# Kernel optimization log

Measured on AMD Instinct MI355X. Metric: run time of the kernel, lower is better.

Reference implementation:

```python
import jax, jax.numpy as jnp
import numpy as np

EMB, CLS, M_MARGIN, B = 512, 20000, 4, 256
LAMB = 1500.0 / 1.1          # AngleLoss lambda at it=1: max(5, 1500/(1+0.1*1))
LMD_INTER = 0.01
PI = 3.14159265              # constant used in original sphereface code


def setup_inputs() -> dict:
    key = jax.random.key(0)
    k1, k2, k3 = jax.random.split(key, 3)
    emb = jax.random.normal(k1, (B, EMB), dtype=jnp.float32)
    y = jax.random.randint(k2, (B,), 0, CLS)
    # weight initialized uniform(-1,1) then column-renormalized inside forward
    W = jax.random.uniform(k3, (EMB, CLS), dtype=jnp.float32, minval=-1.0, maxval=1.0)
    return {"emb": emb, "y": y, "W": W}


def _forward(emb, W, y):
    b = emb.shape[0]
    # --- ASoftmax (sphereface AngleLinear, m=4, phiflag=True) ---
    nm_W = W / jnp.linalg.norm(W, axis=0, keepdims=True)            # unit columns [E,C]
    xlen = jnp.linalg.norm(emb, axis=1, keepdims=True)              # [B,1]
    cos = jnp.clip((emb @ nm_W) / xlen, -1.0, 1.0)                  # [B,C]
    cos_m = 8.0 * cos**4 - 8.0 * cos**2 + 1.0                        # cos(4*theta)
    theta = jnp.arccos(jax.lax.stop_gradient(cos))                   # torch: acos on .data
    k = jnp.floor(M_MARGIN * theta / PI)
    sign = 1.0 - 2.0 * jnp.mod(k, 2.0)                               # (-1)^k
    phi = sign * cos_m - 2.0 * k
    cos_s = cos * xlen                                               # logits[0]
    phi_s = phi * xlen
    # --- AngleLoss (gamma=0) ---
    f = 1.0 / (1.0 + LAMB)
    onehot = jax.nn.one_hot(y, CLS, dtype=cos_s.dtype)               # [B,C]
    output = cos_s + onehot * f * (phi_s - cos_s)
    logpt = jax.nn.log_softmax(output, axis=1)
    logpt_t = jnp.take_along_axis(logpt, y[:, None], axis=1)[:, 0]
    ce = -jnp.mean(logpt_t)
    # --- MHE inter-class loss: sum_{i, j != y_i} 1/||w_{y_i} - w_j||^2 ---
    # unit columns => ||w_a - w_b||^2 = 2 - 2 <w_a, w_b>; avoids the
    # [E, B*C] scatter/repeat intermediate of the original.
    ws = nm_W[:, y]                                                  # [E,B]
    cosWW = ws.T @ nm_W                                              # [B,C]
    dist2 = jnp.maximum(2.0 - 2.0 * cosWW, 0.0)
    mask = onehot > 0.5                                              # j == y_i (z_n == 0)
    inv = jnp.where(mask, 0.0, 1.0 / jnp.where(mask, 1.0, dist2))
    inter = jnp.sum(inv) / (b * (CLS - 1))
    loss = ce + LMD_INTER * inter
    return loss, cos_s, inter


def reference(emb, y, W):
    loss, logits0, inter = _forward(emb, W, y)
    pred = jnp.argmax(logits0, axis=1)
    acc = jnp.mean((pred == y).astype(jnp.float32))
    return loss, logits0, acc, inter
```

## Files before the change

### kernel.cpp

```cpp
#include <hip/hip_runtime.h>
#include <hip/hip_bf16.h>
#include <math.h>

#define B_N   256
#define EMB_N 512
#define CLS_N 20000
#define CLS_PAD 20096
#define NMB   157
#define PI_F  3.14159265f
#define F_CONST ((float)(1.1 / 1501.1))

typedef __bf16 bf16x8 __attribute__((ext_vector_type(8)));
typedef float  f32x4  __attribute__((ext_vector_type(4)));

__device__ __forceinline__ unsigned short f2bf(float f) {
    unsigned u = __float_as_uint(f);
    unsigned r = (u + 0x7FFFu + ((u >> 16) & 1u)) >> 16;
    return (unsigned short)r;
}

__device__ __forceinline__ void merge4(float& M, float& S, float& VM, int& VI,
                                       float m2, float s2, float vm2, int vi2) {
    float mn = fmaxf(M, m2);
    if (mn == -INFINITY) { S = 0.f; }
    else S = S * __expf(M - mn) + s2 * __expf(m2 - mn);
    M = mn;
    if (vm2 > VM || (vm2 == VM && vi2 < VI)) { VM = vm2; VI = vi2; }
}

__device__ __forceinline__ int m204_wgid(int orig) {
    int xcd = orig & 7;
    return (xcd < 4 ? xcd * 79 : 316 + (xcd - 4) * 78) + (orig >> 3);
}

__global__ __launch_bounds__(256) void prep_convert_kernel(
    const float* __restrict__ emb, const int* __restrict__ y,
    const float* __restrict__ W,
    unsigned short* __restrict__ Abf, unsigned short* __restrict__ Wt,
    float* __restrict__ colsumsq4,
    float* __restrict__ xlen_a, float* __restrict__ inv_xlen_a,
    float* __restrict__ inv_wny_a, float* __restrict__ mod_val_a,
    float* __restrict__ accums)
{
    __shared__ alignas(16) unsigned short T[128][136];
    __shared__ float sSq[8][128];
    const int t = threadIdx.x;

    if (blockIdx.x < 628) {
        const int wgid = m204_wgid(blockIdx.x);
        const int c0 = (wgid >> 2) * 128;
        const int k0 = (wgid & 3) * 128;
        const int cl = (t & 31) * 4;
        const int kr = t >> 5;
        const int xp = (t & 7) << 3;
        float ssq[4] = {0.f, 0.f, 0.f, 0.f};

        #pragma unroll 4
        for (int it = 0; it < 16; ++it) {
            int k = k0 + it * 8 + kr;
            int c = c0 + cl;
            float4 v;
            if (c + 3 < CLS_N) {
                v = *reinterpret_cast<const float4*>(&W[(size_t)k * CLS_N + c]);
            } else {
                v.x = (c + 0 < CLS_N) ? W[(size_t)k * CLS_N + c + 0] : 0.f;
                v.y = (c + 1 < CLS_N) ? W[(size_t)k * CLS_N + c + 1] : 0.f;
                v.z = (c + 2 < CLS_N) ? W[(size_t)k * CLS_N + c + 2] : 0.f;
                v.w = (c + 3 < CLS_N) ? W[(size_t)k * CLS_N + c + 3] : 0.f;
            }
            float vv[4] = {v.x, v.y, v.z, v.w};
            int ki = ((it * 8) ^ xp) + kr;
            #pragma unroll
            for (int j = 0; j < 4; ++j) {
                ssq[j] += vv[j] * vv[j];
                T[cl + j][ki] = f2bf(vv[j]);
            }
        }
        #pragma unroll
        for (int j = 0; j < 4; ++j) sSq[kr][cl + j] = 0.f;
        __syncthreads();
        #pragma unroll
        for (int j = 0; j < 4; ++j) atomicAdd(&sSq[kr][cl + j], ssq[j]);
        __syncthreads();
        if (t < 128) {
            float s = 0.f;
            #pragma unroll
            for (int g = 0; g < 8; ++g) s += sSq[g][t];
            colsumsq4[(size_t)(wgid & 3) * CLS_PAD + c0 + t] = s;
        }
        for (int p = 0; p < 8; ++p) {
            int c  = p * 16 + (t >> 4);
            int xr = ((c >> 2) & 7) << 3;
            uint4 d = *reinterpret_cast<const uint4*>(&T[c][((t & 15) * 8) ^ xr]);
            *reinterpret_cast<uint4*>(&Wt[(size_t)(c0 + c) * EMB_N + k0 + (t & 15) * 8]) = d;
        }
    } else {
        float* r0 = (float*)T;
        float* r1 = r0 + 256;
        float* r2 = r0 + 512;
        const int b = blockIdx.x - 628;
        if (b == 0 && t < 4) accums[t] = 0.f;
        const int yb = y[b];
        const float* erow = emb + (size_t)b * EMB_N;
        float se = 0.f, sw = 0.f, dt = 0.f;
        for (int e = t; e < EMB_N; e += 256) {
            float ev = erow[e];
            float wv = W[(size_t)e * CLS_N + yb];
            Abf[(size_t)b * EMB_N + e]         = f2bf(ev);
            Abf[(size_t)(B_N + b) * EMB_N + e] = f2bf(wv);
            se += ev * ev; sw += wv * wv; dt += ev * wv;
        }
        r0[t] = se; r1[t] = sw; r2[t] = dt;
        __syncthreads();
        for (int s = 128; s > 0; s >>= 1) {
            if (t < s) { r0[t] += r0[t + s]; r1[t] += r1[t + s]; r2[t] += r2[t + s]; }
            __syncthreads();
        }
        if (t == 0) {
            float xlen = sqrtf(r0[0]);
            float wn   = sqrtf(r1[0]);
            float inv_x = 1.f / xlen;
            float inv_w = 1.f / wn;
            float cos_t = r2[0] * inv_w * inv_x;
            cos_t = fminf(1.f, fmaxf(-1.f, cos_t));
            float c2 = cos_t * cos_t;
            float cos_m = 8.f * c2 * c2 - 8.f * c2 + 1.f;
            float theta = acosf(cos_t);
            float k = floorf(4.f * theta / PI_F);
            float sgn = 1.f - 2.f * fmodf(k, 2.f);
            float phi = sgn * cos_m - 2.f * k;
            float cos_s = cos_t * xlen;
            float phi_s = phi * xlen;
            xlen_a[b] = xlen;
            inv_xlen_a[b] = inv_x;
            inv_wny_a[b] = inv_w;
            mod_val_a[b] = cos_s + F_CONST * (phi_s - cos_s);
        }
    }
}

__global__ __launch_bounds__(256, 3) void mfma_gemm_kernel(
    const unsigned short* __restrict__ Wt, const unsigned short* __restrict__ Abf,
    const float* __restrict__ colsumsq4, const int* __restrict__ y,
    const float* __restrict__ xlen_a, const float* __restrict__ inv_xlen_a,
    const float* __restrict__ inv_wny_a,
    float* __restrict__ logits, float4* __restrict__ partials,
    float* __restrict__ inter_sum)
{
    __shared__ alignas(16) char smem[49152];
    float*  sIwc  = (float*)smem;
    float4* sPart = (float4*)(smem + 512);
    float*  red   = (float*)(smem + 4608);

    const int wgid = m204_wgid(blockIdx.x);
    const int tile  = wgid >> 2;
    const int slice = wgid & 3;
    const int m0    = tile * 128;
    const int gn0   = slice * 128;

    const int t    = threadIdx.x;
    const int lane = t & 63;
    const int wid  = t >> 6;
    const int wr   = wid >> 1;
    const int wc   = wid & 1;
    const int r16  = lane & 15;
    const int kh   = lane >> 4;

    const char* Ab = (const char*)Wt;
    const char* Bb = (const char*)Abf;

    f32x4 acc[4][4] = {};

    const int srow = lane >> 2;
    const int srcq = (lane & 3) ^ ((lane >> 2) & 3);

    #define ISSUE_STEP(kt, slab)                                                  \
        { _Pragma("unroll")                                                       \
          for (int i = 0; i < 2; ++i) {                                           \
              int slot = wid * 2 + i;                                             \
              int row  = slot * 16 + srow;                                        \
              __builtin_amdgcn_global_load_lds(                                   \
                  (const __attribute__((address_space(1))) unsigned int*)         \
                      (Ab + (size_t)(m0 + row) * 1024                             \
                          + (size_t)(kt) * 2 + srcq * 16),                        \
                  (__attribute__((address_space(3))) unsigned int*)               \
                      (smem + (slab) * 8192 + slot * 1024),                       \
                  16, 0, 0);                                                      \
              __builtin_amdgcn_global_load_lds(                                   \
                  (const __attribute__((address_space(1))) unsigned int*)         \
                      (Bb + (size_t)(gn0 + row) * 1024                            \
                          + (size_t)(kt) * 2 + srcq * 16),                        \
                  (__attribute__((address_space(3))) unsigned int*)               \
                      (smem + 24576 + (slab) * 8192 + slot * 1024),               \
                  16, 0, 0);                                                      \
          } }

    #define COMPUTE(slab)                                                         \
        { bf16x8 af[4], bfr[4];                                                   \
          _Pragma("unroll")                                                       \
          for (int mi = 0; mi < 4; ++mi) {                                        \
              int row = wr * 64 + mi * 16 + r16;                                  \
              af[mi] = *reinterpret_cast<const bf16x8*>(                          \
                  smem + (slab) * 8192 + row * 64 + ((kh ^ (row & 3)) << 4));     \
          }                                                                       \
          _Pragma("unroll")                                                       \
          for (int ni = 0; ni < 4; ++ni) {                                        \
              int rowb = wc * 64 + ni * 16 + r16;                                 \
              bfr[ni] = *reinterpret_cast<const bf16x8*>(                         \
                  smem + 24576 + (slab) * 8192 + rowb * 64                        \
                  + ((kh ^ (rowb & 3)) << 4));                                    \
          }                                                                       \
          __builtin_amdgcn_s_setprio(1);                                          \
          _Pragma("unroll")                                                       \
          for (int mi = 0; mi < 4; ++mi)                                          \
              _Pragma("unroll")                                                   \
              for (int ni = 0; ni < 4; ++ni)                                      \
                  acc[mi][ni] = __builtin_amdgcn_mfma_f32_16x16x32_bf16(          \
                      af[mi], bfr[ni], acc[mi][ni], 0, 0, 0);                     \
          __builtin_amdgcn_s_setprio(0); }

    #define FENCE() __builtin_amdgcn_sched_barrier(0);

    ISSUE_STEP(0, 0)

    #pragma unroll
    for (int tt = 0; tt < 16; ++tt) {
        if (tt < 15) {
            ISSUE_STEP((tt + 1) * 32, (tt + 1) % 3)
            FENCE()
            asm volatile("s_waitcnt vmcnt(4)" ::: "memory");
        } else {
            FENCE()
            asm volatile("s_waitcnt vmcnt(0)" ::: "memory");
        }
        FENCE()
        asm volatile("s_barrier" ::: "memory");
        FENCE()
        COMPUTE(tt % 3)
        FENCE()
    }
    #undef ISSUE_STEP
    #undef COMPUTE
    #undef FENCE

    __syncthreads();

    if (t < 128) {
        int c = m0 + t;
        float s = colsumsq4[c] + colsumsq4[CLS_PAD + c]
                + colsumsq4[2 * CLS_PAD + c] + colsumsq4[3 * CLS_PAD + c];
        sIwc[t] = rsqrtf(s);
    }
    __syncthreads();

    float iwc[4][4];
    #pragma unroll
    for (int mi = 0; mi < 4; ++mi)
        #pragma unroll
        for (int r = 0; r < 4; ++r)
            iwc[mi][r] = sIwc[wr * 64 + mi * 16 + kh * 4 + r];

    if (slice < 2) {
        #pragma unroll
        for (int ni = 0; ni < 4; ++ni) {
            int bl = wc * 64 + ni * 16 + r16;
            int b  = gn0 + bl;
            float xl  = xlen_a[b];
            float ixl = inv_xlen_a[b];
            float M = -INFINITY, S = 0.f, VM = -INFINITY; int VI = 0x7fffffff;
            #pragma unroll
            for (int mi = 0; mi < 4; ++mi) {
                int cb = m0 + wr * 64 + mi * 16 + kh * 4;
                if (cb < CLS_N) {
                    f32x4 vout;
                    #pragma unroll
                    for (int r = 0; r < 4; ++r) {
                        float cosv = acc[mi][ni][r] * iwc[mi][r] * ixl;
                        cosv = fminf(1.f, fmaxf(-1.f, cosv));
                        float v = cosv * xl;
                        vout[r] = v;
                        if (v > M) { S = S * __expf(M - v) + 1.f; M = v; }
                        else       { S += __expf(v - M); }
                        if (v > VM) { VM = v; VI = cb + r; }
                    }
                    *reinterpret_cast<f32x4*>(&logits[(size_t)b * CLS_N + cb]) = vout;
                }
            }
            #pragma unroll
            for (int d = 16; d < 64; d <<= 1) {
                float m2  = __shfl_xor(M, d);
                float s2  = __shfl_xor(S, d);
                float vm2 = __shfl_xor(VM, d);
                int   vi2 = __shfl_xor(VI, d);
                merge4(M, S, VM, VI, m2, s2, vm2, vi2);
            }
            if (kh == 0) sPart[bl * 2 + wr] = make_float4(M, S, VM, __int_as_float(VI));
        }
        __syncthreads();
        if (t < 128) {
            float4 p0 = sPart[t * 2 + 0], p1 = sPart[t * 2 + 1];
            float M = p0.x, S = p0.y, VM = p0.z; int VI = __float_as_int(p0.w);
            merge4(M, S, VM, VI, p1.x, p1.y, p1.z, __float_as_int(p1.w));
            partials[(size_t)(gn0 + t) * NMB + tile] =
                make_float4(M, S, VM, __int_as_float(VI));
        }
    } else {
        float part = 0.f;
        #pragma unroll
        for (int ni = 0; ni < 4; ++ni) {
            int b = (slice - 2) * 128 + wc * 64 + ni * 16 + r16;
            float iwy = inv_wny_a[b];
            int   yb  = y[b];
            #pragma unroll
            for (int mi = 0; mi < 4; ++mi) {
                int cb = m0 + wr * 64 + mi * 16 + kh * 4;
                #pragma unroll
                for (int r = 0; r < 4; ++r) {
                    int c = cb + r;
                    if (c < CLS_N && c != yb) {
                        float cww = acc[mi][ni][r] * iwc[mi][r] * iwy;
                        float d2 = fmaxf(2.f - 2.f * cww, 0.f);
                        part += 1.f / d2;
                    }
                }
            }
        }
        red[t] = part;
        __syncthreads();
        for (int s = 128; s > 0; s >>= 1) {
            if (t < s) red[t] += red[t + s];
            __syncthreads();
        }
        if (t == 0) atomicAdd(inter_sum, red[0]);
    }
}

__global__ __launch_bounds__(64) void reduce_kernel(
    const float4* __restrict__ partials, const float* __restrict__ logits,
    const int* __restrict__ y, const float* __restrict__ mod_val_a,
    float* __restrict__ accums, float* __restrict__ out)
{
    const int b = blockIdx.x;
    const int t = threadIdx.x;
    float M = -INFINITY, S = 0.f, VM = -INFINITY; int VI = 0x7fffffff;
    for (int i = t; i < NMB; i += 64) {
        float4 p = partials[(size_t)b * NMB + i];
        merge4(M, S, VM, VI, p.x, p.y, p.z, __float_as_int(p.w));
    }
    #pragma unroll
    for (int d = 1; d < 64; d <<= 1) {
        float m2  = __shfl_xor(M, d);
        float s2  = __shfl_xor(S, d);
        float vm2 = __shfl_xor(VM, d);
        int   vi2 = __shfl_xor(VI, d);
        merge4(M, S, VM, VI, m2, s2, vm2, vi2);
    }
    if (t == 0) {
        int   yb  = y[b];
        float vyb = logits[(size_t)b * CLS_N + yb];
        float mv  = mod_val_a[b];
        float m2 = fmaxf(M, mv);
        float s2 = S * __expf(M - m2) - __expf(vyb - m2) + __expf(mv - m2);
        float lse = m2 + logf(s2);
        atomicAdd(&accums[0], -(mv - lse));
        if (VI == yb) atomicAdd(&accums[1], 1.f);
        __threadfence();
        int old = atomicAdd((int*)&accums[3], 1);
        if (old == B_N - 1) {
            float ce    = atomicAdd(&accums[0], 0.f) / (float)B_N;
            float acc   = atomicAdd(&accums[1], 0.f) / (float)B_N;
            float inter = atomicAdd(&accums[2], 0.f) / (float)((double)B_N * (CLS_N - 1));
            out[0] = ce + 0.01f * inter;
            out[(size_t)1 + (size_t)B_N * CLS_N + 0] = acc;
            out[(size_t)1 + (size_t)B_N * CLS_N + 1] = inter;
        }
    }
}

extern "C" void kernel_launch(void* const* d_in, const int* in_sizes, int n_in,
                              void* d_out, int out_size, void* d_ws, size_t ws_size,
                              hipStream_t stream) {
    const float* emb = (const float*)d_in[0];
    const int*   y   = (const int*)d_in[1];
    const float* W   = (const float*)d_in[2];
    float* out = (float*)d_out;
    float* logits = out + 1;

    const size_t ABF_OFF  = 0;
    const size_t WT_OFF   = 524288;
    const size_t CS_OFF   = WT_OFF + (size_t)CLS_PAD * EMB_N * 2;
    const size_t PART_OFF = CS_OFF + (size_t)4 * CLS_PAD * 4;
    const size_t SC_OFF   = PART_OFF + (size_t)B_N * NMB * 16;

    unsigned short* Abf = (unsigned short*)((char*)d_ws + ABF_OFF);
    unsigned short* Wt  = (unsigned short*)((char*)d_ws + WT_OFF);
    float*  colsumsq4  = (float*)((char*)d_ws + CS_OFF);
    float4* partials   = (float4*)((char*)d_ws + PART_OFF);
    float*  xlen_a     = (float*)((char*)d_ws + SC_OFF);
    float*  inv_xlen_a = xlen_a + 256;
    float*  inv_wny_a  = xlen_a + 512;
    float*  mod_val_a  = xlen_a + 768;
    float*  accums     = xlen_a + 1024;

    prep_convert_kernel<<<884, 256, 0, stream>>>(emb, y, W, Abf, Wt, colsumsq4,
                                                 xlen_a, inv_xlen_a, inv_wny_a,
                                                 mod_val_a, accums);
    mfma_gemm_kernel<<<628, 256, 0, stream>>>(Wt, Abf, colsumsq4, y,
                                              xlen_a, inv_xlen_a, inv_wny_a,
                                              logits, partials, accums + 2);
    reduce_kernel<<<B_N, 64, 0, stream>>>(partials, logits, y, mod_val_a,
                                          accums, out);
}
```

Baseline: 57.78 us.

## Replace LDS-staged pipelined GEMM with direct-global-load MFMA using 512-thread blocks

Drops the triple-buffered global_load_lds staging and barrier pipeline in the GEMM kernel. Each wave now reads its bf16 A and B fragments directly from global memory (relying on L1/L2) and computes a 32x64 sub-tile instead of 64x64. Workgroups grow to 512 threads (8 waves), and the epilogue reductions are widened to merge four per-row partials. This removes LDS traffic and barrier stalls but gives up explicit LDS reuse and prefetch overlap, so it risks being bound by uncoalesced global or L2 bandwidth.

```diff
diff --git a/kernel.cpp b/kernel.cpp
--- a/kernel.cpp
+++ b/kernel.cpp
@@ -28,7 +28,7 @@
     if (vm2 > VM || (vm2 == VM && vi2 < VI)) { VM = vm2; VI = vi2; }
 }
 
-__device__ __forceinline__ int m204_wgid(int orig) {
+__device__ __forceinline__ int map628(int orig) {
     int xcd = orig & 7;
     return (xcd < 4 ? xcd * 79 : 316 + (xcd - 4) * 78) + (orig >> 3);
 }
@@ -47,7 +47,7 @@
     const int t = threadIdx.x;
 
     if (blockIdx.x < 628) {
-        const int wgid = m204_wgid(blockIdx.x);
+        const int wgid = map628(blockIdx.x);
         const int c0 = (wgid >> 2) * 128;
         const int k0 = (wgid & 3) * 128;
         const int cl = (t & 31) * 4;
@@ -139,7 +139,7 @@
     }
 }
 
-__global__ __launch_bounds__(256, 3) void mfma_gemm_kernel(
+__global__ __launch_bounds__(512) void mfma_gemm_kernel(
     const unsigned short* __restrict__ Wt, const unsigned short* __restrict__ Abf,
     const float* __restrict__ colsumsq4, const int* __restrict__ y,
     const float* __restrict__ xlen_a, const float* __restrict__ inv_xlen_a,
@@ -147,12 +147,11 @@
     float* __restrict__ logits, float4* __restrict__ partials,
     float* __restrict__ inter_sum)
 {
-    __shared__ alignas(16) char smem[49152];
-    float*  sIwc  = (float*)smem;
-    float4* sPart = (float4*)(smem + 512);
-    float*  red   = (float*)(smem + 4608);
-
-    const int wgid = m204_wgid(blockIdx.x);
+    __shared__ float  sIwc[128];
+    __shared__ float4 sPart[128][4];
+    __shared__ float  red[512];
+
+    const int wgid = map628(blockIdx.x);
     const int tile  = wgid >> 2;
     const int slice = wgid & 3;
     const int m0    = tile * 128;
@@ -161,121 +160,65 @@
     const int t    = threadIdx.x;
     const int lane = t & 63;
     const int wid  = t >> 6;
-    const int wr   = wid >> 1;
-    const int wc   = wid & 1;
-    const int r16  = lane & 15;
-    const int kh   = lane >> 4;
-
-    const char* Ab = (const char*)Wt;
-    const char* Bb = (const char*)Abf;
-
-    f32x4 acc[4][4] = {};
-
-    const int srow = lane >> 2;
-    const int srcq = (lane & 3) ^ ((lane >> 2) & 3);
-
-    #define ISSUE_STEP(kt, slab)                                                  \
-        { _Pragma("unroll")                                                       \
-          for (int i = 0; i < 2; ++i) {                                           \
-              int slot = wid * 2 + i;                                             \
-              int row  = slot * 16 + srow;                                        \
-              __builtin_amdgcn_global_load_lds(                                   \
-                  (const __attribute__((address_space(1))) unsigned int*)         \
-                      (Ab + (size_t)(m0 + row) * 1024                             \
-                          + (size_t)(kt) * 2 + srcq * 16),                        \
-                  (__attribute__((address_space(3))) unsigned int*)               \
-                      (smem + (slab) * 8192 + slot * 1024),                       \
-                  16, 0, 0);                                                      \
-              __builtin_amdgcn_global_load_lds(                                   \
-                  (const __attribute__((address_space(1))) unsigned int*)         \
-                      (Bb + (size_t)(gn0 + row) * 1024                            \
-                          + (size_t)(kt) * 2 + srcq * 16),                        \
-                  (__attribute__((address_space(3))) unsigned int*)               \
-                      (smem + 24576 + (slab) * 8192 + slot * 1024),               \
-                  16, 0, 0);                                                      \
-          } }
-
-    #define COMPUTE(slab)                                                         \
-        { bf16x8 af[4], bfr[4];                                                   \
-          _Pragma("unroll")                                                       \
-          for (int mi = 0; mi < 4; ++mi) {                                        \
-              int row = wr * 64 + mi * 16 + r16;                                  \
-              af[mi] = *reinterpret_cast<const bf16x8*>(                          \
-                  smem + (slab) * 8192 + row * 64 + ((kh ^ (row & 3)) << 4));     \
-          }                                                                       \
-          _Pragma("unroll")                                                       \
-          for (int ni = 0; ni < 4; ++ni) {                                        \
-              int rowb = wc * 64 + ni * 16 + r16;                                 \
-              bfr[ni] = *reinterpret_cast<const bf16x8*>(                         \
-                  smem + 24576 + (slab) * 8192 + rowb * 64                        \
-                  + ((kh ^ (rowb & 3)) << 4));                                    \
-          }                                                                       \
-          __builtin_amdgcn_s_setprio(1);                                          \
-          _Pragma("unroll")                                                       \
-          for (int mi = 0; mi < 4; ++mi)                                          \
-              _Pragma("unroll")                                                   \
-              for (int ni = 0; ni < 4; ++ni)                                      \
-                  acc[mi][ni] = __builtin_amdgcn_mfma_f32_16x16x32_bf16(          \
-                      af[mi], bfr[ni], acc[mi][ni], 0, 0, 0);                     \
-          __builtin_amdgcn_s_setprio(0); }
-
-    #define FENCE() __builtin_amdgcn_sched_barrier(0);
-
-    ISSUE_STEP(0, 0)
-
-    #pragma unroll
-    for (int tt = 0; tt < 16; ++tt) {
-        if (tt < 15) {
-            ISSUE_STEP((tt + 1) * 32, (tt + 1) % 3)
-            FENCE()
-            asm volatile("s_waitcnt vmcnt(4)" ::: "memory");
-        } else {
-            FENCE()
-            asm volatile("s_waitcnt vmcnt(0)" ::: "memory");
-        }
-        FENCE()
-        asm volatile("s_barrier" ::: "memory");
-        FENCE()
-        COMPUTE(tt % 3)
-        FENCE()
-    }
-    #undef ISSUE_STEP
-    #undef COMPUTE
-    #undef FENCE
-
-    __syncthreads();
+    const int wcl  = wid >> 1;
+    const int wbh  = wid & 1;
+    const int cl16 = lane & 15;
+    const int k8   = lane >> 4;
+
+    f32x4 acc[2][4] = {};
+
+    const unsigned short* Ap = Wt  + (size_t)(m0 + wcl * 32 + cl16) * EMB_N + k8 * 8;
+    const unsigned short* Bp = Abf + (size_t)(gn0 + wbh * 64 + cl16) * EMB_N + k8 * 8;
+
+    #pragma unroll 4
+    for (int ks = 0; ks < 16; ++ks) {
+        const int kb = ks * 32;
+        bf16x8 af[2], bfr[4];
+        #pragma unroll
+        for (int f = 0; f < 2; ++f)
+            af[f] = *reinterpret_cast<const bf16x8*>(Ap + (size_t)f * 16 * EMB_N + kb);
+        #pragma unroll
+        for (int ni = 0; ni < 4; ++ni)
+            bfr[ni] = *reinterpret_cast<const bf16x8*>(Bp + (size_t)ni * 16 * EMB_N + kb);
+        #pragma unroll
+        for (int f = 0; f < 2; ++f)
+            #pragma unroll
+            for (int ni = 0; ni < 4; ++ni)
+                acc[f][ni] = __builtin_amdgcn_mfma_f32_16x16x32_bf16(
+                    af[f], bfr[ni], acc[f][ni], 0, 0, 0);
+    }
 
     if (t < 128) {
         int c = m0 + t;
         float s = colsumsq4[c] + colsumsq4[CLS_PAD + c]
                 + colsumsq4[2 * CLS_PAD + c] + colsumsq4[3 * CLS_PAD + c];
-        sIwc[t] = rsqrtf(s);
+        sIwc[t] = rsqrtf(fmaxf(s, 1e-30f));
     }
     __syncthreads();
 
-    float iwc[4][4];
+    float iwc[2][4];
     #pragma unroll
-    for (int mi = 0; mi < 4; ++mi)
+    for (int f = 0; f < 2; ++f)
         #pragma unroll
         for (int r = 0; r < 4; ++r)
-            iwc[mi][r] = sIwc[wr * 64 + mi * 16 + kh * 4 + r];
+            iwc[f][r] = sIwc[wcl * 32 + f * 16 + k8 * 4 + r];
 
     if (slice < 2) {
         #pragma unroll
         for (int ni = 0; ni < 4; ++ni) {
-            int bl = wc * 64 + ni * 16 + r16;
+            int bl = wbh * 64 + ni * 16 + cl16;
             int b  = gn0 + bl;
             float xl  = xlen_a[b];
             float ixl = inv_xlen_a[b];
             float M = -INFINITY, S = 0.f, VM = -INFINITY; int VI = 0x7fffffff;
             #pragma unroll
-            for (int mi = 0; mi < 4; ++mi) {
-                int cb = m0 + wr * 64 + mi * 16 + kh * 4;
+            for (int f = 0; f < 2; ++f) {
+                int cb = m0 + wcl * 32 + f * 16 + k8 * 4;
                 if (cb < CLS_N) {
                     f32x4 vout;
                     #pragma unroll
                     for (int r = 0; r < 4; ++r) {
-                        float cosv = acc[mi][ni][r] * iwc[mi][r] * ixl;
+                        float cosv = acc[f][ni][r] * iwc[f][r] * ixl;
                         cosv = fminf(1.f, fmaxf(-1.f, cosv));
                         float v = cosv * xl;
                         vout[r] = v;
@@ -294,13 +237,17 @@
                 int   vi2 = __shfl_xor(VI, d);
                 merge4(M, S, VM, VI, m2, s2, vm2, vi2);
             }
-            if (kh == 0) sPart[bl * 2 + wr] = make_float4(M, S, VM, __int_as_float(VI));
+            if (k8 == 0) sPart[bl][wcl] = make_float4(M, S, VM, __int_as_float(VI));
         }
         __syncthreads();
         if (t < 128) {
-            float4 p0 = sPart[t * 2 + 0], p1 = sPart[t * 2 + 1];
+            float4 p0 = sPart[t][0];
             float M = p0.x, S = p0.y, VM = p0.z; int VI = __float_as_int(p0.w);
-            merge4(M, S, VM, VI, p1.x, p1.y, p1.z, __float_as_int(p1.w));
+            #pragma unroll
+            for (int g = 1; g < 4; ++g) {
+                float4 p = sPart[t][g];
+                merge4(M, S, VM, VI, p.x, p.y, p.z, __float_as_int(p.w));
+            }
             partials[(size_t)(gn0 + t) * NMB + tile] =
                 make_float4(M, S, VM, __int_as_float(VI));
         }
@@ -308,17 +255,17 @@
         float part = 0.f;
         #pragma unroll
         for (int ni = 0; ni < 4; ++ni) {
-            int b = (slice - 2) * 128 + wc * 64 + ni * 16 + r16;
+            int b = (slice - 2) * 128 + wbh * 64 + ni * 16 + cl16;
             float iwy = inv_wny_a[b];
             int   yb  = y[b];
             #pragma unroll
-            for (int mi = 0; mi < 4; ++mi) {
-                int cb = m0 + wr * 64 + mi * 16 + kh * 4;
+            for (int f = 0; f < 2; ++f) {
+                int cb = m0 + wcl * 32 + f * 16 + k8 * 4;
                 #pragma unroll
                 for (int r = 0; r < 4; ++r) {
                     int c = cb + r;
                     if (c < CLS_N && c != yb) {
-                        float cww = acc[mi][ni][r] * iwc[mi][r] * iwy;
+                        float cww = acc[f][ni][r] * iwc[f][r] * iwy;
                         float d2 = fmaxf(2.f - 2.f * cww, 0.f);
                         part += 1.f / d2;
                     }
@@ -327,7 +274,7 @@
         }
         red[t] = part;
         __syncthreads();
-        for (int s = 128; s > 0; s >>= 1) {
+        for (int s = 256; s > 0; s >>= 1) {
             if (t < s) red[t] += red[t + s];
             __syncthreads();
         }
@@ -405,7 +352,7 @@
     prep_convert_kernel<<<884, 256, 0, stream>>>(emb, y, W, Abf, Wt, colsumsq4,
                                                  xlen_a, inv_xlen_a, inv_wny_a,
                                                  mod_val_a, accums);
-    mfma_gemm_kernel<<<628, 256, 0, stream>>>(Wt, Abf, colsumsq4, y,
+    mfma_gemm_kernel<<<628, 512, 0, stream>>>(Wt, Abf, colsumsq4, y,
                                               xlen_a, inv_xlen_a, inv_wny_a,
                                               logits, partials, accums + 2);
     reduce_kernel<<<B_N, 64, 0, stream>>>(partials, logits, y, mod_val_a,
```

Result: slower. 105.3 us (+82.2%).
